# Performance work log

Hardware: AMD Instinct MI355X
Metric: run time of the kernel (lower is better)

## Reference

```python
import jax, jax.numpy as jnp
import numpy as np

V, E, H, T, S = 100000, 256, 512, 48, 2048
HD = H // 2  # per-direction hidden size


def _lstm_dir(x, h0, c0, Wih, Whh, b, reverse):
    # Single-direction LSTM over (S, E) input; PyTorch gate order i,f,g,o.
    def step(carry, xt):
        h, c = carry
        z = xt @ Wih.T + h @ Whh.T + b  # (4*HD,)
        i, f, g, o = jnp.split(z, 4)
        i = jax.nn.sigmoid(i)
        f = jax.nn.sigmoid(f)
        g = jnp.tanh(g)
        o = jax.nn.sigmoid(o)
        c = f * c + i * g
        h = o * jnp.tanh(c)
        return (h, c), h
    _, hs = jax.lax.scan(step, (h0, c0), x, reverse=reverse)
    return hs  # (S, HD)


def setup_inputs() -> dict:
    key = jax.random.key(0)
    ks = jax.random.split(key, 12)
    scale = 1.0 / np.sqrt(HD)
    inp = {
        "sent": jax.random.randint(ks[0], (S,), 0, V),
        "embed_table": jax.random.normal(ks[1], (V, E), jnp.float32),
        "Wih_f": jax.random.normal(ks[2], (4 * HD, E), jnp.float32) * scale,
        "Whh_f": jax.random.normal(ks[3], (4 * HD, HD), jnp.float32) * scale,
        "b_f": jax.random.normal(ks[4], (4 * HD,), jnp.float32) * scale,
        "Wih_b": jax.random.normal(ks[5], (4 * HD, E), jnp.float32) * scale,
        "Whh_b": jax.random.normal(ks[6], (4 * HD, HD), jnp.float32) * scale,
        "b_b": jax.random.normal(ks[7], (4 * HD,), jnp.float32) * scale,
        "W_out": jax.random.normal(ks[8], (T, H), jnp.float32) * (1.0 / np.sqrt(H)),
        "b_out": jnp.zeros((T,), jnp.float32),
        "transitions": jax.random.normal(ks[9], (T, T), jnp.float32) * 0.01,
        "h0": jax.random.normal(ks[10], (2, HD), jnp.float32),
        "c0": jax.random.normal(ks[11], (2, HD), jnp.float32),
    }
    return inp


def reference(sent, embed_table, Wih_f, Whh_f, b_f, Wih_b, Whh_b, b_b,
              W_out, b_out, transitions, h0, c0):
    x = embed_table[sent]  # (S, E)
    hf = _lstm_dir(x, h0[0], c0[0], Wih_f, Whh_f, b_f, False)
    hb = _lstm_dir(x, h0[1], c0[1], Wih_b, Whh_b, b_b, True)
    lstm_out = jnp.concatenate([hf, hb], axis=-1)  # (S, H)
    feats = lstm_out @ W_out.T + b_out  # (S, T) emission scores

    # Viterbi forward pass: scores[i,j] = prev[i] + trans[i,j] + obs[j]
    def vstep(prev, obs):
        scores = prev[:, None] + transitions + obs[None, :]
        return jnp.max(scores, axis=0), jnp.argmax(scores, axis=0)
    prev, bps = jax.lax.scan(vstep, feats[0], feats[1:])  # bps: (S-1, T)

    last = jnp.argmax(prev)

    # Backtrack: reverse scan collects the tag at each timestep in order.
    def back(cur, bp):
        p = bp[cur]
        return p, p
    _, prevs = jax.lax.scan(back, last, bps, reverse=True)  # (S-1,)
    path = jnp.concatenate([prevs, last[None]])  # (S,)
    return path
```

## Files before the change

kernel.cpp:

```cpp
#include <hip/hip_runtime.h>
#include <hip/hip_bf16.h>
#include <math.h>

#define S   2048
#define E   256
#define HD  256
#define NCOL 2048
#define NT  48
#define NWG 16

#define XZ_OFF      ((size_t)0)
#define XZ_BYTES    ((size_t)S * 2048 * 4)
#define LSTM_OFF    (XZ_OFF + XZ_BYTES)
#define LSTM_BYTES  ((size_t)S * 512 * 4)
#define FEATS_OFF   (LSTM_OFF + LSTM_BYTES)
#define FEATS_BYTES ((size_t)S * NT * 4)
#define HCUR2_OFF   (FEATS_OFF + FEATS_BYTES)
#define HCUR2_BYTES ((size_t)2 * 2 * 256 * 8)
#define BPS_OFF     (HCUR2_OFF + HCUR2_BYTES)
#define BPS_BYTES   ((size_t)S * NT)
#define PATHA_OFF   (BPS_OFF + BPS_BYTES)
#define PATHA_BYTES ((size_t)3072 * 32)

__device__ __forceinline__ void st_pair_dev(uint2* p, uint2 v) {
    asm volatile("global_store_dwordx2 %0, %1, off sc0 sc1"
                 :: "v"(p), "v"(v) : "memory");
}

__device__ __forceinline__ bool try_h16(const uint2* p, unsigned want,
                                        float h16[16]) {
    uint4 a, b, c, d, e, f, g, h;
    asm volatile(
        "global_load_dwordx4 %0, %8, off sc0 sc1\n\t"
        "global_load_dwordx4 %1, %8, off offset:16 sc0 sc1\n\t"
        "global_load_dwordx4 %2, %8, off offset:32 sc0 sc1\n\t"
        "global_load_dwordx4 %3, %8, off offset:48 sc0 sc1\n\t"
        "global_load_dwordx4 %4, %8, off offset:64 sc0 sc1\n\t"
        "global_load_dwordx4 %5, %8, off offset:80 sc0 sc1\n\t"
        "global_load_dwordx4 %6, %8, off offset:96 sc0 sc1\n\t"
        "global_load_dwordx4 %7, %8, off offset:112 sc0 sc1\n\t"
        "s_waitcnt vmcnt(0)"
        : "=&v"(a), "=&v"(b), "=&v"(c), "=&v"(d),
          "=&v"(e), "=&v"(f), "=&v"(g), "=&v"(h)
        : "v"(p)
        : "memory");
    const unsigned bad =
        (a.y ^ want) | (a.w ^ want) | (b.y ^ want) | (b.w ^ want) |
        (c.y ^ want) | (c.w ^ want) | (d.y ^ want) | (d.w ^ want) |
        (e.y ^ want) | (e.w ^ want) | (f.y ^ want) | (f.w ^ want) |
        (g.y ^ want) | (g.w ^ want) | (h.y ^ want) | (h.w ^ want);
    if (bad) return false;
    h16[0]  = __uint_as_float(a.x); h16[1]  = __uint_as_float(a.z);
    h16[2]  = __uint_as_float(b.x); h16[3]  = __uint_as_float(b.z);
    h16[4]  = __uint_as_float(c.x); h16[5]  = __uint_as_float(c.z);
    h16[6]  = __uint_as_float(d.x); h16[7]  = __uint_as_float(d.z);
    h16[8]  = __uint_as_float(e.x); h16[9]  = __uint_as_float(e.z);
    h16[10] = __uint_as_float(f.x); h16[11] = __uint_as_float(f.z);
    h16[12] = __uint_as_float(g.x); h16[13] = __uint_as_float(g.z);
    h16[14] = __uint_as_float(h.x); h16[15] = __uint_as_float(h.z);
    return true;
}

__global__ __launch_bounds__(256) void gemm_xz(
    const int* __restrict__ sent, const float* __restrict__ emb,
    const float* __restrict__ Wih_f, const float* __restrict__ Wih_b,
    const float* __restrict__ b_f, const float* __restrict__ b_b,
    float* __restrict__ xz)
{
    __shared__ float As[16][132];
    __shared__ float Bs[16][132];
    const int tid = threadIdx.x;
    const int bm = blockIdx.x * 128;
    const int bn = blockIdx.y * 128;
    const int tx = tid & 15, ty = tid >> 4;
    const int lm = tid >> 1, kq = (tid & 1) * 8;

    const int srow = sent[bm + lm];
    const float* arow = emb + (size_t)srow * E;
    const int bcol = bn + lm;
    const float* brow = (bcol < 1024) ? (Wih_f + (size_t)bcol * E)
                                      : (Wih_b + (size_t)(bcol - 1024) * E);
    float acc[8][8];
#pragma unroll
    for (int i = 0; i < 8; ++i)
#pragma unroll
        for (int j = 0; j < 8; ++j) acc[i][j] = 0.f;

    for (int k0 = 0; k0 < 256; k0 += 16) {
        float4 a0 = *(const float4*)(arow + k0 + kq);
        float4 a1 = *(const float4*)(arow + k0 + kq + 4);
        float4 c0v = *(const float4*)(brow + k0 + kq);
        float4 c1v = *(const float4*)(brow + k0 + kq + 4);
        __syncthreads();
        As[kq + 0][lm] = a0.x; As[kq + 1][lm] = a0.y; As[kq + 2][lm] = a0.z; As[kq + 3][lm] = a0.w;
        As[kq + 4][lm] = a1.x; As[kq + 5][lm] = a1.y; As[kq + 6][lm] = a1.z; As[kq + 7][lm] = a1.w;
        Bs[kq + 0][lm] = c0v.x; Bs[kq + 1][lm] = c0v.y; Bs[kq + 2][lm] = c0v.z; Bs[kq + 3][lm] = c0v.w;
        Bs[kq + 4][lm] = c1v.x; Bs[kq + 5][lm] = c1v.y; Bs[kq + 6][lm] = c1v.z; Bs[kq + 7][lm] = c1v.w;
        __syncthreads();
#pragma unroll
        for (int k = 0; k < 16; ++k) {
            float av[8], bv[8];
            *(float4*)&av[0] = *(const float4*)&As[k][ty * 8];
            *(float4*)&av[4] = *(const float4*)&As[k][ty * 8 + 4];
            *(float4*)&bv[0] = *(const float4*)&Bs[k][tx * 8];
            *(float4*)&bv[4] = *(const float4*)&Bs[k][tx * 8 + 4];
#pragma unroll
            for (int i = 0; i < 8; ++i)
#pragma unroll
                for (int j = 0; j < 8; ++j) acc[i][j] += av[i] * bv[j];
        }
    }
    float bias[8];
    const int cb = bn + tx * 8;
    const float* bptr = (cb < 1024) ? (b_f + cb) : (b_b + cb - 1024);
    *(float4*)&bias[0] = *(const float4*)bptr;
    *(float4*)&bias[4] = *(const float4*)(bptr + 4);
#pragma unroll
    for (int i = 0; i < 8; ++i) {
        const int trow = bm + ty * 8 + i;
        float4 o0, o1;
        o0.x = acc[i][0] + bias[0]; o0.y = acc[i][1] + bias[1];
        o0.z = acc[i][2] + bias[2]; o0.w = acc[i][3] + bias[3];
        o1.x = acc[i][4] + bias[4]; o1.y = acc[i][5] + bias[5];
        o1.z = acc[i][6] + bias[6]; o1.w = acc[i][7] + bias[7];
        *(float4*)(xz + (size_t)trow * NCOL + cb) = o0;
        *(float4*)(xz + (size_t)trow * NCOL + cb + 4) = o1;
    }
}

__global__ void __launch_bounds__(256, 2) lstm_rec(
    const float* __restrict__ Whh_f, const float* __restrict__ Whh_b,
    const float* __restrict__ h0, const float* __restrict__ c0,
    const float* __restrict__ xz, uint2* __restrict__ hcur2,
    float* __restrict__ lstm_out)
{
    __shared__ float red[4][16][8];
    __shared__ float actb[128];
    const int wg = blockIdx.x;
    const int dir = wg >> 3;
    const int wi = wg & 7;
    const int ub = wi * 32;
    const int tid = threadIdx.x;
    const int kg = tid >> 4;
    const int rg = tid & 15;
    const int k0 = kg * 16;
    const float* Whh = dir ? Whh_b : Whh_f;

    float w[8][16];
#pragma unroll
    for (int q = 0; q < 8; ++q) {
        const int lr = rg * 8 + q;
        const int grow = (lr >> 5) * 256 + ub + (lr & 31);
        const float* wr = Whh + (size_t)grow * 256 + k0;
#pragma unroll
        for (int kk = 0; kk < 16; kk += 4) {
            float4 v = *(const float4*)(wr + kk);
            w[q][kk] = v.x; w[q][kk + 1] = v.y; w[q][kk + 2] = v.z; w[q][kk + 3] = v.w;
        }
    }
#pragma unroll
    for (int q = 0; q < 8; ++q)
#pragma unroll
        for (int kk = 0; kk < 16; ++kk)
            asm volatile("" : "+v"(w[q][kk]));

    float cst = 0.f;
    if (tid < 32) {
        cst = c0[dir * 256 + ub + tid];
        uint2 iv;
        iv.x = __float_as_uint(h0[dir * 256 + ub + tid]);
        iv.y = 0u;
        st_pair_dev(hcur2 + (size_t)dir * 256 + ub + tid, iv);
    }
    const int zcol = dir * 1024 + (tid >> 5) * 256 + ub + (tid & 31);

    for (int step = 0; step < S; ++step) {
        float xzv = 0.f;
        if (tid < 128) {
            const int tz = dir ? (S - 1 - step) : step;
            xzv = xz[(size_t)tz * NCOL + zcol];
        }
        const uint2* hb = hcur2 + ((size_t)(step & 1) * 2 + dir) * 256 + k0;
        float h16[16];
        while (!try_h16(hb, (unsigned)step, h16)) {}

        float acc[8];
#pragma unroll
        for (int q = 0; q < 8; ++q) acc[q] = 0.f;
#pragma unroll
        for (int kk = 0; kk < 16; ++kk)
#pragma unroll
            for (int q = 0; q < 8; ++q) acc[q] += w[q][kk] * h16[kk];
#pragma unroll
        for (int q = 0; q < 8; ++q) {
            acc[q] += __shfl_xor(acc[q], 16);
            acc[q] += __shfl_xor(acc[q], 32);
        }
        if ((kg & 3) == 0) {
            const int wv = kg >> 2;
#pragma unroll
            for (int q = 0; q < 8; ++q) red[wv][rg][q] = acc[q];
        }
        __syncthreads();
        if (tid < 128) {
            const int rg2 = tid >> 3, q2 = tid & 7;
            const float z = ((red[0][rg2][q2] + red[1][rg2][q2]) +
                             (red[2][rg2][q2] + red[3][rg2][q2])) + xzv;
            const int gate = tid >> 5;
            actb[tid] = (gate == 2) ? tanhf(z) : (1.f / (1.f + expf(-z)));
        }
        __syncthreads();
        if (tid < 32) {
            const int u = tid;
            const float ig = actb[u];
            const float fg = actb[32 + u];
            const float gg = actb[64 + u];
            const float og = actb[96 + u];
            cst = fg * cst + ig * gg;
            const float h = og * tanhf(cst);
            const int tz = dir ? (S - 1 - step) : step;
            uint2 pv;
            pv.x = __float_as_uint(h);
            pv.y = (unsigned)(step + 1);
            st_pair_dev(hcur2 + ((size_t)((step + 1) & 1) * 2 + dir) * 256 + ub + u, pv);
            lstm_out[(size_t)tz * 512 + dir * 256 + ub + u] = h;
        }
    }
}

__global__ __launch_bounds__(256) void feats_k(
    const float* __restrict__ lstm, const float* __restrict__ Wout,
    const float* __restrict__ bout, float* __restrict__ feats)
{
    const int gid = blockIdx.x * 256 + threadIdx.x;
    if (gid >= S * NT) return;
    const int t = gid / NT, tag = gid - t * NT;
    const float* hr = lstm + (size_t)t * 512;
    const float* wr = Wout + (size_t)tag * 512;
    float s0 = 0, s1 = 0, s2 = 0, s3 = 0;
#pragma unroll 4
    for (int k = 0; k < 512; k += 4) {
        float4 h4 = *(const float4*)(hr + k);
        float4 w4 = *(const float4*)(wr + k);
        s0 += h4.x * w4.x; s1 += h4.y * w4.y;
        s2 += h4.z * w4.z; s3 += h4.w * w4.w;
    }
    feats[gid] = (s0 + s1) + (s2 + s3) + bout[tag];
}

__global__ void __launch_bounds__(256, 1) viterbi_k(
    const float* __restrict__ feats, const float* __restrict__ trans,
    unsigned char* __restrict__ bps, unsigned char* __restrict__ pathA,
    int* __restrict__ out)
{
    __shared__ float v2[2][NT];
    __shared__ unsigned char cmap[64][NT];
    __shared__ int SB[65];
    __shared__ int last_s;
    const int tid = threadIdx.x;
    const int j = tid >> 2, ig = tid & 3;
    const bool act = (tid < 192);

    float Treg[12];
    if (act) {
#pragma unroll
        for (int r = 0; r < 12; ++r) Treg[r] = trans[(ig * 12 + r) * NT + j];
    }
    if (tid < NT) v2[0][tid] = feats[tid];
    __syncthreads();

    float obs_c = 0.f;
    if (act) obs_c = feats[NT + j];
    for (int t = 1; t < S; ++t) {
        float obs_n = 0.f;
        if (act && t < S - 1) obs_n = feats[(size_t)(t + 1) * NT + j];
        const int p = (t - 1) & 1;
        if (act) {
            float best = -1e30f; int bi = 0;
#pragma unroll
            for (int r = 0; r < 12; ++r) {
                const int i = ig * 12 + r;
                const float sc = (v2[p][i] + Treg[r]) + obs_c;
                if (sc > best) { best = sc; bi = i; }
            }
            {
                float ob = __shfl_xor(best, 1); int obi = __shfl_xor(bi, 1);
                if (ob > best || (ob == best && obi < bi)) { best = ob; bi = obi; }
                ob = __shfl_xor(best, 2); obi = __shfl_xor(bi, 2);
                if (ob > best || (ob == best && obi < bi)) { best = ob; bi = obi; }
            }
            if (ig == 0) {
                v2[p ^ 1][j] = best;
                bps[(size_t)(t - 1) * NT + j] = (unsigned char)bi;
            }
        }
        __syncthreads();
        obs_c = obs_n;
    }
    if (tid == 0) {
        float b = -1e30f; int bi = 0;
        for (int q = 0; q < NT; ++q) { if (v2[1][q] > b) { b = v2[1][q]; bi = q; } }
        last_s = bi;
    }
    int cArr[12], sArr[12];
    unsigned char stv[12];
#pragma unroll
    for (int r = 0; r < 12; ++r) {
        const int task = r * 256 + tid;
        cArr[r] = task / NT;
        sArr[r] = task - cArr[r] * NT;
        stv[r] = (unsigned char)sArr[r];
    }
    for (int stp = 31; stp >= 0; --stp) {
#pragma unroll
        for (int r = 0; r < 12; ++r) {
            const int km = cArr[r] * 32 + stp;
            if (km < S - 1) stv[r] = bps[(size_t)km * NT + stv[r]];
            pathA[(size_t)(cArr[r] * NT + sArr[r]) * 32 + stp] = stv[r];
        }
    }
#pragma unroll
    for (int r = 0; r < 12; ++r) cmap[cArr[r]][sArr[r]] = stv[r];
    __syncthreads();
    if (tid == 0) {
        SB[64] = last_s;
        for (int c = 63; c >= 0; --c) SB[c] = cmap[c][SB[c + 1]];
    }
    __syncthreads();
    for (int t = tid; t < S; t += 256) {
        const int c = t >> 5;
        out[t] = (int)pathA[(size_t)(c * NT + SB[c + 1]) * 32 + (t & 31)];
    }
}

extern "C" void kernel_launch(void* const* d_in, const int* in_sizes, int n_in,
                              void* d_out, int out_size, void* d_ws, size_t ws_size,
                              hipStream_t stream) {
    const int*   sent   = (const int*)d_in[0];
    const float* emb    = (const float*)d_in[1];
    const float* Wih_f  = (const float*)d_in[2];
    const float* Whh_f  = (const float*)d_in[3];
    const float* b_f    = (const float*)d_in[4];
    const float* Wih_b  = (const float*)d_in[5];
    const float* Whh_b  = (const float*)d_in[6];
    const float* b_b    = (const float*)d_in[7];
    const float* W_out  = (const float*)d_in[8];
    const float* b_out  = (const float*)d_in[9];
    const float* trans  = (const float*)d_in[10];
    const float* h0     = (const float*)d_in[11];
    const float* c0     = (const float*)d_in[12];
    int* out = (int*)d_out;

    char* ws = (char*)d_ws;
    float* xz       = (float*)(ws + XZ_OFF);
    float* lstm     = (float*)(ws + LSTM_OFF);
    float* feats    = (float*)(ws + FEATS_OFF);
    uint2* hcur2    = (uint2*)(ws + HCUR2_OFF);
    unsigned char* bps   = (unsigned char*)(ws + BPS_OFF);
    unsigned char* pathA = (unsigned char*)(ws + PATHA_OFF);

    hipMemsetAsync(hcur2, 0xFF, HCUR2_BYTES, stream);

    gemm_xz<<<dim3(16, 16), 256, 0, stream>>>(sent, emb, Wih_f, Wih_b, b_f, b_b, xz);

    lstm_rec<<<dim3(NWG), 256, 0, stream>>>(Whh_f, Whh_b, h0, c0, xz, hcur2, lstm);

    feats_k<<<dim3((S * NT + 255) / 256), 256, 0, stream>>>(lstm, W_out, b_out, feats);

    viterbi_k<<<dim3(1), 256, 0, stream>>>(feats, trans, bps, pathA, out);
}
```

Baseline: 5.654 ms.

## Remap LSTM recurrence so each wave owns whole units, removing block barriers

The recurrent kernel's thread mapping changes so that each wavefront owns 8 hidden units across all four gates. The k-dimension reduction now uses intra-wave shuffles and gate values are exchanged via shuffles instead of shared memory, which removes both __syncthreads per timestep. Each wave publishes its own h slice directly and writes lstm_out as float4. Launch bounds drop to 1 block per CU. In exchange, activation math is now redundant across lanes and there are more shuffle operations per step.

New measurement: 11.12 ms. 1.97x slower.

```diff
diff --git a/kernel.cpp b/kernel.cpp
--- a/kernel.cpp
+++ b/kernel.cpp
@@ -128,102 +128,129 @@
     }
 }
 
-__global__ void __launch_bounds__(256, 2) lstm_rec(
+__global__ void __launch_bounds__(256, 1) lstm_rec(
     const float* __restrict__ Whh_f, const float* __restrict__ Whh_b,
     const float* __restrict__ h0, const float* __restrict__ c0,
     const float* __restrict__ xz, uint2* __restrict__ hcur2,
     float* __restrict__ lstm_out)
 {
-    __shared__ float red[4][16][8];
-    __shared__ float actb[128];
-    const int wg = blockIdx.x;
-    const int dir = wg >> 3;
-    const int wi = wg & 7;
-    const int ub = wi * 32;
-    const int tid = threadIdx.x;
-    const int kg = tid >> 4;
-    const int rg = tid & 15;
-    const int k0 = kg * 16;
+    const int wg   = blockIdx.x;
+    const int dir  = wg >> 3;
+    const int wi   = wg & 7;
+    const int tid  = threadIdx.x;
+    const int wave = tid >> 6;
+    const int lane = tid & 63;
+    const int kg   = lane & 15;
+    const int rg   = lane >> 4;
+    const int k0   = kg * 16;
+    const int ug   = wi * 32 + wave * 8;
     const float* Whh = dir ? Whh_b : Whh_f;
 
     float w[8][16];
 #pragma unroll
     for (int q = 0; q < 8; ++q) {
-        const int lr = rg * 8 + q;
-        const int grow = (lr >> 5) * 256 + ub + (lr & 31);
-        const float* wr = Whh + (size_t)grow * 256 + k0;
+        const float* wr = Whh + (size_t)(rg * 256 + ug + q) * 256 + k0;
 #pragma unroll
         for (int kk = 0; kk < 16; kk += 4) {
             float4 v = *(const float4*)(wr + kk);
             w[q][kk] = v.x; w[q][kk + 1] = v.y; w[q][kk + 2] = v.z; w[q][kk + 3] = v.w;
         }
     }
-#pragma unroll
-    for (int q = 0; q < 8; ++q)
+
+    float c[8];
+#pragma unroll
+    for (int q = 0; q < 8; ++q) c[q] = 0.f;
+    if (rg == 0) {
+#pragma unroll
+        for (int q = 0; q < 8; ++q) c[q] = c0[dir * 256 + ug + q];
+    }
+
+    if (rg == 0 && kg < 8) {
+        uint2 iv;
+        iv.x = __float_as_uint(h0[dir * 256 + ug + kg]);
+        iv.y = 0u;
+        st_pair_dev(hcur2 + (size_t)dir * 256 + ug + kg, iv);
+    }
+
+    for (int step = 0; step < S; ++step) {
+#pragma unroll
+        for (int q = 0; q < 8; ++q)
+            asm volatile("" : "+v"(w[q][0]), "+v"(w[q][1]), "+v"(w[q][2]), "+v"(w[q][3]),
+                              "+v"(w[q][4]), "+v"(w[q][5]), "+v"(w[q][6]), "+v"(w[q][7]),
+                              "+v"(w[q][8]), "+v"(w[q][9]), "+v"(w[q][10]), "+v"(w[q][11]),
+                              "+v"(w[q][12]), "+v"(w[q][13]), "+v"(w[q][14]), "+v"(w[q][15]));
+
+        const int tz = dir ? (S - 1 - step) : step;
+        const float* xp = xz + (size_t)tz * NCOL + dir * 1024 + rg * 256 + ug;
+        float4 x0 = *(const float4*)xp;
+        float4 x1 = *(const float4*)(xp + 4);
+
+        const uint2* hb = hcur2 + ((size_t)(step & 1) * 2 + dir) * 256 + k0;
+        float hv[16];
+        while (!try_h16(hb, (unsigned)step, hv)) {}
+
+        float acc[8];
+#pragma unroll
+        for (int q = 0; q < 8; ++q) acc[q] = 0.f;
 #pragma unroll
         for (int kk = 0; kk < 16; ++kk)
-            asm volatile("" : "+v"(w[q][kk]));
-
-    float cst = 0.f;
-    if (tid < 32) {
-        cst = c0[dir * 256 + ub + tid];
-        uint2 iv;
-        iv.x = __float_as_uint(h0[dir * 256 + ub + tid]);
-        iv.y = 0u;
-        st_pair_dev(hcur2 + (size_t)dir * 256 + ub + tid, iv);
-    }
-    const int zcol = dir * 1024 + (tid >> 5) * 256 + ub + (tid & 31);
-
-    for (int step = 0; step < S; ++step) {
-        float xzv = 0.f;
-        if (tid < 128) {
-            const int tz = dir ? (S - 1 - step) : step;
-            xzv = xz[(size_t)tz * NCOL + zcol];
-        }
-        const uint2* hb = hcur2 + ((size_t)(step & 1) * 2 + dir) * 256 + k0;
-        float h16[16];
-        while (!try_h16(hb, (unsigned)step, h16)) {}
-
-        float acc[8];
-#pragma unroll
-        for (int q = 0; q < 8; ++q) acc[q] = 0.f;
-#pragma unroll
-        for (int kk = 0; kk < 16; ++kk)
-#pragma unroll
-            for (int q = 0; q < 8; ++q) acc[q] += w[q][kk] * h16[kk];
+#pragma unroll
+            for (int q = 0; q < 8; ++q) acc[q] += w[q][kk] * hv[kk];
 #pragma unroll
         for (int q = 0; q < 8; ++q) {
-            acc[q] += __shfl_xor(acc[q], 16);
-            acc[q] += __shfl_xor(acc[q], 32);
-        }
-        if ((kg & 3) == 0) {
-            const int wv = kg >> 2;
-#pragma unroll
-            for (int q = 0; q < 8; ++q) red[wv][rg][q] = acc[q];
-        }
-        __syncthreads();
-        if (tid < 128) {
-            const int rg2 = tid >> 3, q2 = tid & 7;
-            const float z = ((red[0][rg2][q2] + red[1][rg2][q2]) +
-                             (red[2][rg2][q2] + red[3][rg2][q2])) + xzv;
-            const int gate = tid >> 5;
-            actb[tid] = (gate == 2) ? tanhf(z) : (1.f / (1.f + expf(-z)));
-        }
-        __syncthreads();
-        if (tid < 32) {
-            const int u = tid;
-            const float ig = actb[u];
-            const float fg = actb[32 + u];
-            const float gg = actb[64 + u];
-            const float og = actb[96 + u];
-            cst = fg * cst + ig * gg;
-            const float h = og * tanhf(cst);
-            const int tz = dir ? (S - 1 - step) : step;
-            uint2 pv;
-            pv.x = __float_as_uint(h);
-            pv.y = (unsigned)(step + 1);
-            st_pair_dev(hcur2 + ((size_t)((step + 1) & 1) * 2 + dir) * 256 + ub + u, pv);
-            lstm_out[(size_t)tz * 512 + dir * 256 + ub + u] = h;
+            acc[q] += __shfl_xor(acc[q], 1);
+            acc[q] += __shfl_xor(acc[q], 2);
+            acc[q] += __shfl_xor(acc[q], 4);
+            acc[q] += __shfl_xor(acc[q], 8);
+        }
+        float z[8];
+        z[0] = acc[0] + x0.x; z[1] = acc[1] + x0.y;
+        z[2] = acc[2] + x0.z; z[3] = acc[3] + x0.w;
+        z[4] = acc[4] + x1.x; z[5] = acc[5] + x1.y;
+        z[6] = acc[6] + x1.z; z[7] = acc[7] + x1.w;
+        float av[8];
+        if (rg == 2) {
+#pragma unroll
+            for (int q = 0; q < 8; ++q) av[q] = tanhf(z[q]);
+        } else {
+#pragma unroll
+            for (int q = 0; q < 8; ++q) av[q] = 1.f / (1.f + expf(-z[q]));
+        }
+        float gf[8], gg[8], go[8];
+#pragma unroll
+        for (int q = 0; q < 8; ++q) {
+            gf[q] = __shfl_xor(av[q], 16);
+            gg[q] = __shfl_xor(av[q], 32);
+            go[q] = __shfl_xor(av[q], 48);
+        }
+        float h[8];
+#pragma unroll
+        for (int q = 0; q < 8; ++q) h[q] = 0.f;
+        if (rg == 0) {
+#pragma unroll
+            for (int q = 0; q < 8; ++q) {
+                c[q] = gf[q] * c[q] + av[q] * gg[q];
+                h[q] = go[q] * tanhf(c[q]);
+            }
+        }
+        if (rg == 0) {
+            float myh = h[0];
+#pragma unroll
+            for (int q = 1; q < 8; ++q) myh = (kg == q) ? h[q] : myh;
+            if (kg < 8) {
+                uint2 pv;
+                pv.x = __float_as_uint(myh);
+                pv.y = (unsigned)(step + 1);
+                st_pair_dev(hcur2 + ((size_t)((step + 1) & 1) * 2 + dir) * 256 + ug + kg, pv);
+            }
+        }
+        if (lane == 0) {
+            float4 o0, o1;
+            o0.x = h[0]; o0.y = h[1]; o0.z = h[2]; o0.w = h[3];
+            o1.x = h[4]; o1.y = h[5]; o1.z = h[6]; o1.w = h[7];
+            float* lp = lstm_out + (size_t)tz * 512 + dir * 256 + ug;
+            *(float4*)lp = o0;
+            *(float4*)(lp + 4) = o1;
         }
     }
 }
```

## Interleave gate rows so LSTM cell update uses shuffles instead of a barrier

Applied to the files above, without the earlier changes.

Reorders the Whh rows held by each thread so the four gates of one hidden unit sit in adjacent lanes. The gate activations can then be combined with wave shuffles instead of going through shared memory and a second __syncthreads per step. The reduction buffer is double-buffered by step parity so the next step's writes cannot race with this step's reads. Launch bounds drop to one block per SIMD target, which may change register allocation for the 128-float weight cache.

Result: slower. 6.393 ms (+13.1%).

```diff
diff --git a/kernel.cpp b/kernel.cpp
--- a/kernel.cpp
+++ b/kernel.cpp
@@ -128,14 +128,13 @@
     }
 }
 
-__global__ void __launch_bounds__(256, 2) lstm_rec(
+__global__ void __launch_bounds__(256, 1) lstm_rec(
     const float* __restrict__ Whh_f, const float* __restrict__ Whh_b,
     const float* __restrict__ h0, const float* __restrict__ c0,
     const float* __restrict__ xz, uint2* __restrict__ hcur2,
     float* __restrict__ lstm_out)
 {
-    __shared__ float red[4][16][8];
-    __shared__ float actb[128];
+    __shared__ float red[2][4][16][8];
     const int wg = blockIdx.x;
     const int dir = wg >> 3;
     const int wi = wg & 7;
@@ -150,7 +149,7 @@
 #pragma unroll
     for (int q = 0; q < 8; ++q) {
         const int lr = rg * 8 + q;
-        const int grow = (lr >> 5) * 256 + ub + (lr & 31);
+        const int grow = (lr & 3) * 256 + ub + (lr >> 2);
         const float* wr = Whh + (size_t)grow * 256 + k0;
 #pragma unroll
         for (int kk = 0; kk < 16; kk += 4) {
@@ -164,23 +163,27 @@
         for (int kk = 0; kk < 16; ++kk)
             asm volatile("" : "+v"(w[q][kk]));
 
+    const int gate = tid & 3;
+    const int uu   = tid >> 2;
+    const bool lead = (tid < 128) && (gate == 0);
+
     float cst = 0.f;
-    if (tid < 32) {
-        cst = c0[dir * 256 + ub + tid];
+    if (lead) {
+        cst = c0[dir * 256 + ub + uu];
         uint2 iv;
-        iv.x = __float_as_uint(h0[dir * 256 + ub + tid]);
+        iv.x = __float_as_uint(h0[dir * 256 + ub + uu]);
         iv.y = 0u;
-        st_pair_dev(hcur2 + (size_t)dir * 256 + ub + tid, iv);
-    }
-    const int zcol = dir * 1024 + (tid >> 5) * 256 + ub + (tid & 31);
+        st_pair_dev(hcur2 + (size_t)dir * 256 + ub + uu, iv);
+    }
+    const int zcol = dir * 1024 + gate * 256 + ub + uu;
 
     for (int step = 0; step < S; ++step) {
+        const int p = step & 1;
+        const int tz = dir ? (S - 1 - step) : step;
         float xzv = 0.f;
-        if (tid < 128) {
-            const int tz = dir ? (S - 1 - step) : step;
-            xzv = xz[(size_t)tz * NCOL + zcol];
-        }
-        const uint2* hb = hcur2 + ((size_t)(step & 1) * 2 + dir) * 256 + k0;
+        if (tid < 128) xzv = xz[(size_t)tz * NCOL + zcol];
+
+        const uint2* hb = hcur2 + ((size_t)p * 2 + dir) * 256 + k0;
         float h16[16];
         while (!try_h16(hb, (unsigned)step, h16)) {}
 
@@ -199,31 +202,26 @@
         if ((kg & 3) == 0) {
             const int wv = kg >> 2;
 #pragma unroll
-            for (int q = 0; q < 8; ++q) red[wv][rg][q] = acc[q];
+            for (int q = 0; q < 8; ++q) red[p][wv][rg][q] = acc[q];
         }
         __syncthreads();
         if (tid < 128) {
             const int rg2 = tid >> 3, q2 = tid & 7;
-            const float z = ((red[0][rg2][q2] + red[1][rg2][q2]) +
-                             (red[2][rg2][q2] + red[3][rg2][q2])) + xzv;
-            const int gate = tid >> 5;
-            actb[tid] = (gate == 2) ? tanhf(z) : (1.f / (1.f + expf(-z)));
-        }
-        __syncthreads();
-        if (tid < 32) {
-            const int u = tid;
-            const float ig = actb[u];
-            const float fg = actb[32 + u];
-            const float gg = actb[64 + u];
-            const float og = actb[96 + u];
-            cst = fg * cst + ig * gg;
-            const float h = og * tanhf(cst);
-            const int tz = dir ? (S - 1 - step) : step;
-            uint2 pv;
-            pv.x = __float_as_uint(h);
-            pv.y = (unsigned)(step + 1);
-            st_pair_dev(hcur2 + ((size_t)((step + 1) & 1) * 2 + dir) * 256 + ub + u, pv);
-            lstm_out[(size_t)tz * 512 + dir * 256 + ub + u] = h;
+            const float z = ((red[p][0][rg2][q2] + red[p][1][rg2][q2]) +
+                             (red[p][2][rg2][q2] + red[p][3][rg2][q2])) + xzv;
+            const float av = (gate == 2) ? tanhf(z) : (1.f / (1.f + expf(-z)));
+            const float fg = __shfl_xor(av, 1);
+            const float gg = __shfl_xor(av, 2);
+            const float og = __shfl_xor(av, 3);
+            if (gate == 0) {
+                cst = fg * cst + av * gg;
+                const float h = og * tanhf(cst);
+                uint2 pv;
+                pv.x = __float_as_uint(h);
+                pv.y = (unsigned)(step + 1);
+                st_pair_dev(hcur2 + ((size_t)((step + 1) & 1) * 2 + dir) * 256 + ub + uu, pv);
+                lstm_out[(size_t)tz * 512 + dir * 256 + ub + uu] = h;
+            }
         }
     }
 }
```
